# Optimization experiments

Hardware: AMD Instinct MI355X
Metric: run time of the kernel (lower is better)

The kernel has to match this reference:

```python
import jax, jax.numpy as jnp
import numpy as np

STATE_DIM = 1024
INPUT_DIM = 1024
OUTPUT_DIM = 1024
BATCH = 8
SEQ = 2048


def setup_inputs() -> dict:
    key = jax.random.key(0)
    k_x, k_a, k_b, k_w, k_bias = jax.random.split(key, 5)
    x = jax.random.normal(k_x, (BATCH, SEQ, INPUT_DIM), dtype=jnp.float32)
    # diagonal transition a in (0, 0.99) for stability
    A = jax.random.uniform(k_a, (STATE_DIM,), dtype=jnp.float32, minval=0.0, maxval=0.99)
    B = jax.random.normal(k_b, (STATE_DIM, INPUT_DIM), dtype=jnp.float32) / np.sqrt(INPUT_DIM)
    W = jax.random.normal(k_w, (OUTPUT_DIM, STATE_DIM), dtype=jnp.float32) / np.sqrt(STATE_DIM)
    b = jax.random.normal(k_bias, (OUTPUT_DIM,), dtype=jnp.float32) * 0.01
    return {"x": x, "A": A, "B": B, "W": W, "b": b}


def reference(x, A, B, W, b):
    # x: [batch, seq, input_dim]
    # Input projection: u_t = B x_t  -> [batch, seq, state_dim]
    u = jnp.einsum('bld,nd->bln', x, B)
    # Diagonal linear recurrence h_t = A * h_{t-1} + u_t via associative scan.
    # Pair representation (a, b) composes as (a1*a2, a2*b1 + b2).
    aa = jnp.broadcast_to(A, u.shape)

    def combine(c1, c2):
        a1, b1 = c1
        a2, b2 = c2
        return a1 * a2, a2 * b1 + b2

    _, h = jax.lax.associative_scan(combine, (aa, u), axis=1)
    # Output projection: [batch, seq, output_dim]
    return jnp.einsum('bln,on->blo', h, W) + b
```

## Files before the change

### kernel.cpp

```cpp
#include <hip/hip_runtime.h>
#include <stdint.h>

#define BATCH 8
#define SEQ 2048
#define DIM 1024
#define MTOT (BATCH * SEQ)

typedef __attribute__((ext_vector_type(8))) short short8;
typedef __attribute__((ext_vector_type(8))) unsigned short ushort8;
typedef __attribute__((ext_vector_type(4))) float floatx4;


__device__ __forceinline__ unsigned short f2bf(float f) {
  union { float f; unsigned u; } c; c.f = f;
  unsigned u = c.u;
  return (unsigned short)((u + 0x7FFFu + ((u >> 16) & 1u)) >> 16);
}
__device__ __forceinline__ float bf2f(unsigned short h) {
  union { unsigned u; float f; } c; c.u = ((unsigned)h) << 16;
  return c.f;
}

__device__ __forceinline__ void gll16(const void* g, void* l) {
  __builtin_amdgcn_global_load_lds(
      (__attribute__((address_space(1))) void*)(uintptr_t)g,
      (__attribute__((address_space(3))) void*)(uintptr_t)l,
      16, 0, 0);
}


#define X4 (MTOT * DIM / 4)
#define M4 (DIM * DIM / 4)

__global__ __launch_bounds__(256) void cast3_kernel(
    const float* __restrict__ x, const float* __restrict__ B,
    const float* __restrict__ W, unsigned short* __restrict__ xb,
    unsigned short* __restrict__ Bb, unsigned short* __restrict__ Wb) {
  int i = blockIdx.x * 256 + threadIdx.x;
  const float4* s4;
  uint2* d2;
  int li;
  if (i < X4) {
    s4 = (const float4*)x; d2 = (uint2*)xb; li = i;
  } else if (i < X4 + M4) {
    s4 = (const float4*)B; d2 = (uint2*)Bb; li = i - X4;
  } else {
    s4 = (const float4*)W; d2 = (uint2*)Wb; li = i - X4 - M4;
  }
  float4 v = s4[li];
  uint2 o;
  o.x = (unsigned)f2bf(v.x) | ((unsigned)f2bf(v.y) << 16);
  o.y = (unsigned)f2bf(v.z) | ((unsigned)f2bf(v.w) << 16);
  d2[li] = o;
}


__global__ __launch_bounds__(256) void gemm1_fused(
    const unsigned short* __restrict__ A,
    const unsigned short* __restrict__ B,
    unsigned short* __restrict__ u,
    const float* __restrict__ Adiag,
    float* __restrict__ aggbuf) {
  __shared__ unsigned short smem[16384];
  __shared__ float segsum[2][128];
  unsigned short* sA = smem;
  unsigned short* sB = smem + 8192;

  const int tid = threadIdx.x;
  const int wave = tid >> 6, lane = tid & 63;

  const int id = blockIdx.x;
  const int xcd = id & 7, j = id >> 3;
  const int mt = xcd * 16 + (j >> 3);
  const int nt = j & 7;
  const size_t m0 = (size_t)mt * 128;
  const int n0 = nt * 128;

  floatx4 acc[4][4] = {};

  const int srow = wave * 8 + (lane >> 3);
  const int scol = (((lane & 7) ^ ((lane >> 3) & 7)) * 8);
  const unsigned short* gA = A + (m0 + srow) * 1024 + scol;
  const unsigned short* gB = B + ((size_t)n0 + srow) * 1024 + scol;
  unsigned short* lA = sA + wave * 8 * 64;
  unsigned short* lB = sB + wave * 8 * 64;

  const int fr = lane & 15;
  const int frs = fr & 7;
  const int kb = lane >> 4;
  const int wm = (wave & 1) * 64, wn = (wave >> 1) * 64;

  for (int kt = 0; kt < 1024; kt += 64) {
#pragma unroll
    for (int r = 0; r < 4; ++r) {
      gll16(gA + (size_t)r * 32 * 1024 + kt, lA + r * 32 * 64);
      gll16(gB + (size_t)r * 32 * 1024 + kt, lB + r * 32 * 64);
    }
    asm volatile("s_waitcnt vmcnt(0)" ::: "memory");
    __syncthreads();
#pragma unroll
    for (int kk = 0; kk < 64; kk += 32) {
      short8 af[4], bfv[4];
#pragma unroll
      for (int i = 0; i < 4; ++i)
        af[i] = *(const short8*)(sA + (wm + i * 16 + fr) * 64 +
                                 ((((kk >> 3) + kb) ^ frs) * 8));
#pragma unroll
      for (int jj = 0; jj < 4; ++jj)
        bfv[jj] = *(const short8*)(sB + (wn + jj * 16 + fr) * 64 +
                                   ((((kk >> 3) + kb) ^ frs) * 8));
#pragma unroll
      for (int i = 0; i < 4; ++i)
#pragma unroll
        for (int jj = 0; jj < 4; ++jj)
          acc[i][jj] = __builtin_amdgcn_mfma_f32_16x16x32_bf16(
              af[i], bfv[jj], acc[i][jj], 0, 0, 0);
    }
    __syncthreads();
  }

  const int col = lane & 15;
  const int row4 = (lane >> 4) * 4;
  unsigned short* sC = smem;
#pragma unroll
  for (int i = 0; i < 4; ++i)
#pragma unroll
    for (int jj = 0; jj < 4; ++jj)
#pragma unroll
      for (int r = 0; r < 4; ++r)
        sC[(wm + i * 16 + row4 + r) * 128 + wn + jj * 16 + col] =
            f2bf(acc[i][jj][r]);
  __syncthreads();

  const int colv = tid & 127;
  const int seg = tid >> 7;
  const float a = Adiag[n0 + colv];
  {
    float s = 0.f;
    const int t0 = seg * 64;
#pragma unroll 8
    for (int t = 0; t < 64; ++t) {
      int idx = (t0 + t) * 128 + colv;
      s = fmaf(a, s, bf2f(sC[idx]));
      sC[idx] = f2bf(s);
    }
    segsum[seg][colv] = s;
  }
  __syncthreads();

  {
    float a2 = a * a, a4 = a2 * a2, a8 = a4 * a4, a16 = a8 * a8;
    float a32 = a16 * a16, a64 = a32 * a32;
    const float s0 = segsum[0][colv];
    const int t0 = 64 + seg * 32;
    float apow = seg ? a32 * a : a;
#pragma unroll 8
    for (int t = 0; t < 32; ++t) {
      int idx = (t0 + t) * 128 + colv;
      sC[idx] = f2bf(fmaf(apow, s0, bf2f(sC[idx])));
      apow *= a;
    }
    if (seg)
      aggbuf[(size_t)mt * 1024 + n0 + colv] =
          fmaf(a64, s0, segsum[1][colv]);
  }
  __syncthreads();

#pragma unroll
  for (int s = 0; s < 8; ++s) {
    int row = wave * 32 + s * 4 + (lane >> 4);
    int c8 = (lane & 15) * 8;
    *(ushort8*)(u + (m0 + row) * (size_t)1024 + n0 + c8) =
        *(const ushort8*)(sC + row * 128 + c8);
  }
}


__global__ __launch_bounds__(256) void combine_kernel(
    const float* __restrict__ agg, float* __restrict__ carry,
    const float* __restrict__ Adiag) {
  const int id = blockIdx.x * 256 + threadIdx.x;
  const int b = id >> 10, n = id & (DIM - 1);
  float a = Adiag[n];
  float aL = a;
#pragma unroll
  for (int i = 0; i < 7; ++i) aL *= aL;
  float s = 0.f;
#pragma unroll
  for (int c = 0; c < 16; ++c) {
    size_t idx = (size_t)(b * 16 + c) * 1024 + n;
    float local = agg[idx];
    carry[idx] = s;
    s = fmaf(aL, s, local);
  }
}


__global__ __launch_bounds__(256) void apply_kernel(
    unsigned short* __restrict__ u, const float* __restrict__ Adiag,
    const float* __restrict__ carry) {
  const int id = blockIdx.x;
  const int xcd = id & 7, rem = id >> 3;
  const int mt = xcd * 16 + (rem >> 4);
  const int sub = rem & 15;
  const int tg = threadIdx.x >> 7;
  const int ch0 = (threadIdx.x & 127) * 8;

  float a[8], cf[8];
  *(float4*)&a[0] = *(const float4*)(Adiag + ch0);
  *(float4*)&a[4] = *(const float4*)(Adiag + ch0 + 4);
  const float* cp = carry + (size_t)mt * 1024 + ch0;
  *(float4*)&cf[0] = *(const float4*)cp;
  *(float4*)&cf[4] = *(const float4*)(cp + 4);

  const int tl = sub * 8 + tg * 4;
  float apow[8];
#pragma unroll
  for (int j = 0; j < 8; ++j)
    apow[j] = __builtin_amdgcn_exp2f(__builtin_amdgcn_logf(a[j]) *
                                     (float)(tl + 1));
  const size_t base = ((size_t)mt * 128 + tl) * DIM + ch0;
#pragma unroll
  for (int s = 0; s < 4; ++s) {
    ushort8 v = *(const ushort8*)(u + base + (size_t)s * DIM);
    ushort8 o;
#pragma unroll
    for (int j = 0; j < 8; ++j) {
      o[j] = f2bf(fmaf(apow[j], cf[j], bf2f(v[j])));
      apow[j] *= a[j];
    }
    *(ushort8*)(u + base + (size_t)s * DIM) = o;
  }
}


__global__ __launch_bounds__(256) void gemm2(
    const unsigned short* __restrict__ A, const unsigned short* __restrict__ B,
    float* __restrict__ C, const float* __restrict__ bias) {
  __shared__ unsigned short smem[16384];
  unsigned short* sA = smem;
  unsigned short* sB = smem + 8192;

  const int tid = threadIdx.x;
  const int wave = tid >> 6, lane = tid & 63;

  const int id = blockIdx.x;
  const int xcd = id & 7, j = id >> 3;
  const int mt = xcd * 16 + (j >> 3);
  const int nt = j & 7;
  const size_t m0 = (size_t)mt * 128;
  const int n0 = nt * 128;

  floatx4 acc[4][4] = {};

  const int srow = wave * 8 + (lane >> 3);
  const int scol = (((lane & 7) ^ ((lane >> 3) & 7)) * 8);
  const unsigned short* gA = A + (m0 + srow) * 1024 + scol;
  const unsigned short* gB = B + ((size_t)n0 + srow) * 1024 + scol;
  unsigned short* lA = sA + wave * 8 * 64;
  unsigned short* lB = sB + wave * 8 * 64;

  const int fr = lane & 15;
  const int frs = fr & 7;
  const int kb = lane >> 4;
  const int wm = (wave & 1) * 64, wn = (wave >> 1) * 64;

  for (int kt = 0; kt < 1024; kt += 64) {
#pragma unroll
    for (int r = 0; r < 4; ++r) {
      gll16(gA + (size_t)r * 32 * 1024 + kt, lA + r * 32 * 64);
      gll16(gB + (size_t)r * 32 * 1024 + kt, lB + r * 32 * 64);
    }
    asm volatile("s_waitcnt vmcnt(0)" ::: "memory");
    __syncthreads();
#pragma unroll
    for (int kk = 0; kk < 64; kk += 32) {
      short8 af[4], bfv[4];
#pragma unroll
      for (int i = 0; i < 4; ++i)
        af[i] = *(const short8*)(sA + (wm + i * 16 + fr) * 64 +
                                 ((((kk >> 3) + kb) ^ frs) * 8));
#pragma unroll
      for (int jj = 0; jj < 4; ++jj)
        bfv[jj] = *(const short8*)(sB + (wn + jj * 16 + fr) * 64 +
                                   ((((kk >> 3) + kb) ^ frs) * 8));
#pragma unroll
      for (int i = 0; i < 4; ++i)
#pragma unroll
        for (int jj = 0; jj < 4; ++jj)
          acc[i][jj] = __builtin_amdgcn_mfma_f32_16x16x32_bf16(
              af[i], bfv[jj], acc[i][jj], 0, 0, 0);
    }
    __syncthreads();
  }

  const int col = lane & 15;
  const int row4 = (lane >> 4) * 4;
#pragma unroll
  for (int i = 0; i < 4; ++i)
#pragma unroll
    for (int jj = 0; jj < 4; ++jj)
#pragma unroll
      for (int r = 0; r < 4; ++r) {
        size_t m = m0 + wm + i * 16 + row4 + r;
        int n = n0 + wn + jj * 16 + col;
        C[m * 1024 + n] = acc[i][jj][r] + bias[n];
      }
}


extern "C" void kernel_launch(void* const* d_in, const int* in_sizes, int n_in,
                              void* d_out, int out_size, void* d_ws,
                              size_t ws_size, hipStream_t stream) {
  const float* x    = (const float*)d_in[0];
  const float* A    = (const float*)d_in[1];
  const float* B    = (const float*)d_in[2];
  const float* W    = (const float*)d_in[3];
  const float* bias = (const float*)d_in[4];

  char* ws = (char*)d_ws;
  unsigned short* xb   = (unsigned short*)ws;
  unsigned short* ubuf = (unsigned short*)(ws + 33554432);
  unsigned short* Bb   = (unsigned short*)(ws + 67108864);
  unsigned short* Wb   = (unsigned short*)(ws + 69206016);
  float* aggbuf        = (float*)(ws + 71303168);
  float* carry         = (float*)(ws + 71827456);

  cast3_kernel<<<(X4 + 2 * M4) / 256, 256, 0, stream>>>(x, B, W, xb, Bb, Wb);

  gemm1_fused<<<1024, 256, 0, stream>>>(xb, Bb, ubuf, A, aggbuf);

  combine_kernel<<<32, 256, 0, stream>>>(aggbuf, carry, A);

  apply_kernel<<<2048, 256, 0, stream>>>(ubuf, A, carry);

  gemm2<<<1024, 256, 0, stream>>>(ubuf, Wb, (float*)d_out, bias);
}
```

Baseline: 233.5 us.

## Fuse x bf16 cast into GEMM1 A-load and fold carry combine into apply

The separate pass that cast the large activation tensor x to bf16 is removed. GEMM1 now loads fp32 x directly, converts it with a truncating byte-perm pack, and writes the bf16 values into swizzled LDS, while B is still fetched with async global-to-LDS loads. The combine kernel is also dropped: each apply block recomputes its own carry serially from the per-chunk aggregates. This saves a full write and re-read of bf16 x plus one launch, but GEMM1 now reads twice the A bytes per tile and goes through registers for them, and the pack truncates rather than rounds.

```diff
diff --git a/kernel.cpp b/kernel.cpp
--- a/kernel.cpp
+++ b/kernel.cpp
@@ -28,25 +28,23 @@
       16, 0, 0);
 }
 
-
-#define X4 (MTOT * DIM / 4)
+__device__ __forceinline__ unsigned pkbf(float f1, float f0) {
+  return __builtin_amdgcn_perm(__builtin_bit_cast(unsigned, f1),
+                               __builtin_bit_cast(unsigned, f0), 0x07060302u);
+}
+
+
 #define M4 (DIM * DIM / 4)
 
-__global__ __launch_bounds__(256) void cast3_kernel(
-    const float* __restrict__ x, const float* __restrict__ B,
-    const float* __restrict__ W, unsigned short* __restrict__ xb,
+__global__ __launch_bounds__(256) void castBW_kernel(
+    const float* __restrict__ B, const float* __restrict__ W,
     unsigned short* __restrict__ Bb, unsigned short* __restrict__ Wb) {
   int i = blockIdx.x * 256 + threadIdx.x;
   const float4* s4;
   uint2* d2;
   int li;
-  if (i < X4) {
-    s4 = (const float4*)x; d2 = (uint2*)xb; li = i;
-  } else if (i < X4 + M4) {
-    s4 = (const float4*)B; d2 = (uint2*)Bb; li = i - X4;
-  } else {
-    s4 = (const float4*)W; d2 = (uint2*)Wb; li = i - X4 - M4;
-  }
+  if (i < M4) { s4 = (const float4*)B; d2 = (uint2*)Bb; li = i; }
+  else        { s4 = (const float4*)W; d2 = (uint2*)Wb; li = i - M4; }
   float4 v = s4[li];
   uint2 o;
   o.x = (unsigned)f2bf(v.x) | ((unsigned)f2bf(v.y) << 16);
@@ -56,8 +54,8 @@
 
 
 __global__ __launch_bounds__(256) void gemm1_fused(
-    const unsigned short* __restrict__ A,
-    const unsigned short* __restrict__ B,
+    const float* __restrict__ x,
+    const unsigned short* __restrict__ Bb,
     unsigned short* __restrict__ u,
     const float* __restrict__ Adiag,
     float* __restrict__ aggbuf) {
@@ -78,11 +76,20 @@
 
   floatx4 acc[4][4] = {};
 
+  const int arow = tid >> 2;
+  const int ak0 = (tid & 3) * 16;
+  const float* gx0 = x + (m0 + arow) * 1024 + ak0;
+  const float* gx1 = x + (m0 + 64 + arow) * 1024 + ak0;
+  const int ablk = (tid & 3) * 2;
+  char* sAc = (char*)sA;
+  const unsigned la0a = (unsigned)(arow * 128 + ((ablk ^ (arow & 7)) * 16));
+  const unsigned la0b = (unsigned)(arow * 128 + (((ablk + 1) ^ (arow & 7)) * 16));
+  const unsigned la1a = (unsigned)((64 + arow) * 128 + ((ablk ^ (arow & 7)) * 16));
+  const unsigned la1b = (unsigned)((64 + arow) * 128 + (((ablk + 1) ^ (arow & 7)) * 16));
+
   const int srow = wave * 8 + (lane >> 3);
   const int scol = (((lane & 7) ^ ((lane >> 3) & 7)) * 8);
-  const unsigned short* gA = A + (m0 + srow) * 1024 + scol;
-  const unsigned short* gB = B + ((size_t)n0 + srow) * 1024 + scol;
-  unsigned short* lA = sA + wave * 8 * 64;
+  const unsigned short* gB = Bb + ((size_t)n0 + srow) * 1024 + scol;
   unsigned short* lB = sB + wave * 8 * 64;
 
   const int fr = lane & 15;
@@ -92,10 +99,30 @@
 
   for (int kt = 0; kt < 1024; kt += 64) {
 #pragma unroll
-    for (int r = 0; r < 4; ++r) {
-      gll16(gA + (size_t)r * 32 * 1024 + kt, lA + r * 32 * 64);
+    for (int r = 0; r < 4; ++r)
       gll16(gB + (size_t)r * 32 * 1024 + kt, lB + r * 32 * 64);
-    }
+
+    float4 f0 = *(const float4*)(gx0 + kt);
+    float4 f1 = *(const float4*)(gx0 + kt + 4);
+    float4 f2 = *(const float4*)(gx0 + kt + 8);
+    float4 f3 = *(const float4*)(gx0 + kt + 12);
+    float4 f4 = *(const float4*)(gx1 + kt);
+    float4 f5 = *(const float4*)(gx1 + kt + 4);
+    float4 f6 = *(const float4*)(gx1 + kt + 8);
+    float4 f7 = *(const float4*)(gx1 + kt + 12);
+    uint4 w0 = {pkbf(f0.y, f0.x), pkbf(f0.w, f0.z),
+                pkbf(f1.y, f1.x), pkbf(f1.w, f1.z)};
+    uint4 w1 = {pkbf(f2.y, f2.x), pkbf(f2.w, f2.z),
+                pkbf(f3.y, f3.x), pkbf(f3.w, f3.z)};
+    uint4 w2 = {pkbf(f4.y, f4.x), pkbf(f4.w, f4.z),
+                pkbf(f5.y, f5.x), pkbf(f5.w, f5.z)};
+    uint4 w3 = {pkbf(f6.y, f6.x), pkbf(f6.w, f6.z),
+                pkbf(f7.y, f7.x), pkbf(f7.w, f7.z)};
+    *(uint4*)(sAc + la0a) = w0;
+    *(uint4*)(sAc + la0b) = w1;
+    *(uint4*)(sAc + la1a) = w2;
+    *(uint4*)(sAc + la1b) = w3;
+
     asm volatile("s_waitcnt vmcnt(0)" ::: "memory");
     __syncthreads();
 #pragma unroll
@@ -161,8 +188,7 @@
       apow *= a;
     }
     if (seg)
-      aggbuf[(size_t)mt * 1024 + n0 + colv] =
-          fmaf(a64, s0, segsum[1][colv]);
+      aggbuf[(size_t)mt * 1024 + n0 + colv] = fmaf(a64, s0, segsum[1][colv]);
   }
   __syncthreads();
 
@@ -176,42 +202,39 @@
 }
 
 
-__global__ __launch_bounds__(256) void combine_kernel(
-    const float* __restrict__ agg, float* __restrict__ carry,
-    const float* __restrict__ Adiag) {
-  const int id = blockIdx.x * 256 + threadIdx.x;
-  const int b = id >> 10, n = id & (DIM - 1);
-  float a = Adiag[n];
-  float aL = a;
-#pragma unroll
-  for (int i = 0; i < 7; ++i) aL *= aL;
-  float s = 0.f;
-#pragma unroll
-  for (int c = 0; c < 16; ++c) {
-    size_t idx = (size_t)(b * 16 + c) * 1024 + n;
-    float local = agg[idx];
-    carry[idx] = s;
-    s = fmaf(aL, s, local);
-  }
-}
-
-
 __global__ __launch_bounds__(256) void apply_kernel(
     unsigned short* __restrict__ u, const float* __restrict__ Adiag,
-    const float* __restrict__ carry) {
+    const float* __restrict__ aggbuf) {
   const int id = blockIdx.x;
   const int xcd = id & 7, rem = id >> 3;
   const int mt = xcd * 16 + (rem >> 4);
   const int sub = rem & 15;
   const int tg = threadIdx.x >> 7;
   const int ch0 = (threadIdx.x & 127) * 8;
-
-  float a[8], cf[8];
+  const int b = mt >> 4, c = mt & 15;
+
+  float a[8];
   *(float4*)&a[0] = *(const float4*)(Adiag + ch0);
   *(float4*)&a[4] = *(const float4*)(Adiag + ch0 + 4);
-  const float* cp = carry + (size_t)mt * 1024 + ch0;
-  *(float4*)&cf[0] = *(const float4*)cp;
-  *(float4*)&cf[4] = *(const float4*)(cp + 4);
+  float aL[8];
+#pragma unroll
+  for (int j = 0; j < 8; ++j) {
+    float t = a[j];
+    t *= t; t *= t; t *= t; t *= t; t *= t; t *= t; t *= t;
+    aL[j] = t;
+  }
+
+  float cf[8];
+#pragma unroll
+  for (int j = 0; j < 8; ++j) cf[j] = 0.f;
+  const float* ab = aggbuf + (size_t)(b * 16) * 1024 + ch0;
+  for (int p = 0; p < c; ++p) {
+    float4 g0 = *(const float4*)(ab + (size_t)p * 1024);
+    float4 g1 = *(const float4*)(ab + (size_t)p * 1024 + 4);
+    float g[8] = {g0.x, g0.y, g0.z, g0.w, g1.x, g1.y, g1.z, g1.w};
+#pragma unroll
+    for (int j = 0; j < 8; ++j) cf[j] = fmaf(aL[j], cf[j], g[j]);
+  }
 
   const int tl = sub * 8 + tg * 4;
   float apow[8];
@@ -319,20 +342,16 @@
   const float* bias = (const float*)d_in[4];
 
   char* ws = (char*)d_ws;
-  unsigned short* xb   = (unsigned short*)ws;
-  unsigned short* ubuf = (unsigned short*)(ws + 33554432);
-  unsigned short* Bb   = (unsigned short*)(ws + 67108864);
-  unsigned short* Wb   = (unsigned short*)(ws + 69206016);
-  float* aggbuf        = (float*)(ws + 71303168);
-  float* carry         = (float*)(ws + 71827456);
-
-  cast3_kernel<<<(X4 + 2 * M4) / 256, 256, 0, stream>>>(x, B, W, xb, Bb, Wb);
-
-  gemm1_fused<<<1024, 256, 0, stream>>>(xb, Bb, ubuf, A, aggbuf);
-
-  combine_kernel<<<32, 256, 0, stream>>>(aggbuf, carry, A);
-
-  apply_kernel<<<2048, 256, 0, stream>>>(ubuf, A, carry);
+  unsigned short* ubuf = (unsigned short*)ws;
+  unsigned short* Bb   = (unsigned short*)(ws + 33554432);
+  unsigned short* Wb   = (unsigned short*)(ws + 35651584);
+  float* aggbuf        = (float*)(ws + 37748736);
+
+  castBW_kernel<<<2 * M4 / 256, 256, 0, stream>>>(B, W, Bb, Wb);
+
+  gemm1_fused<<<1024, 256, 0, stream>>>(x, Bb, ubuf, A, aggbuf);
+
+  apply_kernel<<<2048, 256, 0, stream>>>(ubuf, A, aggbuf);
 
   gemm2<<<1024, 256, 0, stream>>>(ubuf, Wb, (float*)d_out, bias);
 }
```

Measured after the change: 237.4 us. Within noise of the previous version (+1.7%).
